# Kernel tuning notes

Measured on AMD Instinct MI355X. Metric: run time of the kernel, lower is better.

## Reference

```python
import jax, jax.numpy as jnp
import numpy as np

N_NODES = 100000
N_EDGES = 1600000
HEADS = 4
HID = 32
NEG_SLOPE = 0.2
EPS = 1e-16


def _gat_layer(x, w, a_src, a_dst, b, src, dst, n_nodes, concat):
    # x: [N, F_in], w: [H*C, F_in], a_src/a_dst: [H, C]
    H, C = a_src.shape
    h = (x @ w.T).reshape(-1, H, C)                      # [N, H, C]
    alpha_src = jnp.einsum('nhc,hc->nh', h, a_src)       # [N, H]
    alpha_dst = jnp.einsum('nhc,hc->nh', h, a_dst)       # [N, H]
    e = alpha_src[src] + alpha_dst[dst]                  # [E, H]
    e = jax.nn.leaky_relu(e, NEG_SLOPE)
    # segment softmax over incoming edges of each dst node
    m = jax.ops.segment_max(e, dst, num_segments=n_nodes)   # [N, H]
    ex = jnp.exp(e - m[dst])
    denom = jax.ops.segment_sum(ex, dst, num_segments=n_nodes)  # [N, H]
    alpha = ex / (denom[dst] + EPS)                      # [E, H]
    msg = alpha[:, :, None] * h[src]                     # [E, H, C]
    out = jax.ops.segment_sum(msg, dst, num_segments=n_nodes)  # [N, H, C]
    if concat:
        out = out.reshape(n_nodes, H * C)
    else:
        out = out.mean(axis=1)
    return out + b


def setup_inputs() -> dict:
    key = jax.random.key(0)
    ks = jax.random.split(key, 16)
    x = jax.random.normal(ks[0], (N_NODES, 3), dtype=jnp.float32)
    edge_index = jax.random.randint(ks[1], (2, N_EDGES), 0, N_NODES, dtype=jnp.int64 if jax.config.read('jax_enable_x64') else jnp.int32)
    s = 0.1
    return {
        'x': x,
        'edge_index': edge_index,
        'w1': jax.random.normal(ks[2], (HEADS * HID, 3)) * s,
        'att_src1': jax.random.normal(ks[3], (HEADS, HID)) * s,
        'att_dst1': jax.random.normal(ks[4], (HEADS, HID)) * s,
        'b1': jax.random.normal(ks[5], (HEADS * HID,)) * s,
        'w2': jax.random.normal(ks[6], (HID, HEADS * HID)) * s,
        'att_src2': jax.random.normal(ks[7], (1, HID)) * s,
        'att_dst2': jax.random.normal(ks[8], (1, HID)) * s,
        'b2': jax.random.normal(ks[9], (HID,)) * s,
        'mlp_w1': jax.random.normal(ks[10], (HID, 2 * HID)) * s,
        'mlp_b1': jax.random.normal(ks[11], (HID,)) * s,
        'mlp_w2': jax.random.normal(ks[12], (1, HID)) * s,
        'mlp_b2': jax.random.normal(ks[13], (1,)) * s,
    }


def reference(x, edge_index, w1, att_src1, att_dst1, b1, w2, att_src2, att_dst2, b2,
              mlp_w1, mlp_b1, mlp_w2, mlp_b2):
    src, dst = edge_index[0], edge_index[1]
    n = x.shape[0]
    # dropout layers are identity in eval mode
    h = _gat_layer(x, w1, att_src1, att_dst1, b1, src, dst, n, concat=True)   # [N, H*C]
    h = jax.nn.elu(h)
    h = _gat_layer(h, w2, att_src2, att_dst2, b2, src, dst, n, concat=False)  # [N, C]
    ef = jnp.concatenate([h[src], h[dst]], axis=-1)                            # [E, 2C]
    ef = jax.nn.relu(ef @ mlp_w1.T + mlp_b1)
    flows = (ef @ mlp_w2.T + mlp_b2).squeeze(-1)                               # [E]
    return jax.nn.relu(flows)
```

## Files before the change

### kernel.cpp

```cpp
#include <hip/hip_runtime.h>
#include <hip/hip_fp16.h>
#include <math.h>

#define N_NODES 100000
#define N_EDGES 1600000
#define NEG_SLOPE 0.2f
#define EPS 1e-16f

#define NBUCK 196
#define CHUNK 4096
#define BLKB 391

__device__ __forceinline__ float lrelu(float v) { return v > 0.f ? v : NEG_SLOPE * v; }

__device__ __forceinline__ float4 ld4h(const __half* p) {
    uint2 r = *(const uint2*)p;
    __half2 h0 = *reinterpret_cast<const __half2*>(&r.x);
    __half2 h1 = *reinterpret_cast<const __half2*>(&r.y);
    float2 f0 = __half22float2(h0), f1 = __half22float2(h1);
    return make_float4(f0.x, f0.y, f1.x, f1.y);
}

__device__ __forceinline__ void ld8h(const __half* p, float* f) {
    uint4 r = *(const uint4*)p;
    __half2 h0 = *reinterpret_cast<const __half2*>(&r.x);
    __half2 h1 = *reinterpret_cast<const __half2*>(&r.y);
    __half2 h2 = *reinterpret_cast<const __half2*>(&r.z);
    __half2 h3 = *reinterpret_cast<const __half2*>(&r.w);
    float2 f0 = __half22float2(h0), f1 = __half22float2(h1);
    float2 f2 = __half22float2(h2), f3 = __half22float2(h3);
    f[0] = f0.x; f[1] = f0.y; f[2] = f1.x; f[3] = f1.y;
    f[4] = f2.x; f[5] = f2.y; f[6] = f3.x; f[7] = f3.y;
}

__global__ void kA_hist(const int* __restrict__ ei, int* __restrict__ bh) {
    __shared__ int hist[NBUCK];
    int tid = threadIdx.x, b = blockIdx.x;
    if (tid < NBUCK) hist[tid] = 0;
    __syncthreads();
    int base = b * CHUNK;
    #pragma unroll
    for (int i = 0; i < CHUNK / 256; i++) {
        int e = base + i * 256 + tid;
        if (e < N_EDGES) {
            int dst = ei[N_EDGES + e];
            atomicAdd(&hist[dst >> 9], 1);
        }
    }
    __syncthreads();
    if (tid < NBUCK) bh[b * NBUCK + tid] = hist[tid];
}

__global__ void kS1(int* __restrict__ bh, int* __restrict__ bucketStart) {
    __shared__ int tsum[256];
    int k = blockIdx.x, t = threadIdx.x;
    int j0 = 2 * t, j1 = 2 * t + 1;
    int v0 = (j0 < BLKB) ? bh[j0 * NBUCK + k] : 0;
    int v1 = (j1 < BLKB) ? bh[j1 * NBUCK + k] : 0;
    int s = v0 + v1;
    tsum[t] = s;
    __syncthreads();
    for (int off = 1; off < 256; off <<= 1) {
        int tv = (t >= off) ? tsum[t - off] : 0;
        __syncthreads();
        tsum[t] += tv;
        __syncthreads();
    }
    int excl = tsum[t] - s;
    if (j0 < BLKB) bh[j0 * NBUCK + k] = excl;
    if (j1 < BLKB) bh[j1 * NBUCK + k] = excl + v0;
    if (t == 255) bucketStart[k] = tsum[255];
}

__global__ void kS2(int* __restrict__ bucketStart) {
    __shared__ int tmp[256];
    int t = threadIdx.x;
    int v = (t < NBUCK) ? bucketStart[t] : 0;
    tmp[t] = v;
    __syncthreads();
    for (int off = 1; off < 256; off <<= 1) {
        int tv = (t >= off) ? tmp[t - off] : 0;
        __syncthreads();
        tmp[t] += tv;
        __syncthreads();
    }
    if (t < NBUCK) bucketStart[t] = tmp[t] - v;
    if (t == NBUCK - 1) bucketStart[NBUCK] = tmp[t];
}

__global__ void kB_bin(const int* __restrict__ ei, const int* __restrict__ bh,
                       const int* __restrict__ bucketStart, int* __restrict__ binned) {
    __shared__ int cur[NBUCK];
    int tid = threadIdx.x, b = blockIdx.x;
    if (tid < NBUCK) cur[tid] = bucketStart[tid] + bh[b * NBUCK + tid];
    __syncthreads();
    int base = b * CHUNK;
    #pragma unroll
    for (int i = 0; i < CHUNK / 256; i++) {
        int e = base + i * 256 + tid;
        if (e < N_EDGES) {
            int src = ei[e], dst = ei[N_EDGES + e];
            int pos = atomicAdd(&cur[dst >> 9], 1);
            binned[pos] = src | ((dst & 511) << 17);
        }
    }
}

__global__ void kC_sort(const int* __restrict__ bucketStart, const int* __restrict__ binned,
                        int* __restrict__ deg, int* __restrict__ rowptr,
                        int* __restrict__ csr_src) {
    __shared__ int cnt[512];
    __shared__ int pfx[512];
    __shared__ int bsum[256];
    int t = threadIdx.x, k = blockIdx.x;
    int s0 = bucketStart[k], s1 = bucketStart[k + 1];
    cnt[t] = 0; cnt[t + 256] = 0;
    __syncthreads();
    for (int i = s0 + t; i < s1; i += 256)
        atomicAdd(&cnt[binned[i] >> 17], 1);
    __syncthreads();
    int a0 = cnt[2 * t], a1 = cnt[2 * t + 1];
    int s = a0 + a1;
    bsum[t] = s;
    __syncthreads();
    for (int off = 1; off < 256; off <<= 1) {
        int tv = (t >= off) ? bsum[t - off] : 0;
        __syncthreads();
        bsum[t] += tv;
        __syncthreads();
    }
    int excl = bsum[t] - s;
    pfx[2 * t] = excl;
    pfx[2 * t + 1] = excl + a0;
    int nb0 = k << 9;
    int n0 = nb0 + 2 * t, n1 = nb0 + 2 * t + 1;
    if (n0 < N_NODES) { deg[n0] = a0; rowptr[n0] = s0 + excl; }
    if (n1 < N_NODES) { deg[n1] = a1; rowptr[n1] = s0 + excl + a0; }
    __syncthreads();
    for (int i = s0 + t; i < s1; i += 256) {
        int pkd = binned[i];
        int pos = s0 + atomicAdd(&pfx[pkd >> 17], 1);
        csr_src[pos] = pkd & 0x1FFFF;
    }
}

__global__ void k_q(const float* __restrict__ w1, const float* __restrict__ as1,
                    const float* __restrict__ ad1, float* __restrict__ qv) {
    int t = threadIdx.x;
    if (t >= 24) return;
    int c = t % 3, h = (t / 3) % 4, side = t / 12;
    const float* att = side ? ad1 : as1;
    float acc = 0.f;
    for (int cc = 0; cc < 32; cc++)
        acc += att[h * 32 + cc] * w1[(h * 32 + cc) * 3 + c];
    qv[t] = acc;
}

__global__ void k_node1(const float* __restrict__ x, const float* __restrict__ qv,
                        float* __restrict__ a1d, float* __restrict__ p1) {
    int n = blockIdx.x * blockDim.x + threadIdx.x;
    if (n >= N_NODES) return;
    float x0 = x[n * 3], x1 = x[n * 3 + 1], x2 = x[n * 3 + 2];
    float4 s, d;
    s.x = x0 * qv[0]  + x1 * qv[1]  + x2 * qv[2];
    s.y = x0 * qv[3]  + x1 * qv[4]  + x2 * qv[5];
    s.z = x0 * qv[6]  + x1 * qv[7]  + x2 * qv[8];
    s.w = x0 * qv[9]  + x1 * qv[10] + x2 * qv[11];
    d.x = x0 * qv[12] + x1 * qv[13] + x2 * qv[14];
    d.y = x0 * qv[15] + x1 * qv[16] + x2 * qv[17];
    d.z = x0 * qv[18] + x1 * qv[19] + x2 * qv[20];
    d.w = x0 * qv[21] + x1 * qv[22] + x2 * qv[23];
    ((float4*)a1d)[n] = d;
    ((float4*)p1)[n * 2]     = s;
    float4 xx; xx.x = x0; xx.y = x1; xx.z = x2; xx.w = 1.f;
    ((float4*)p1)[n * 2 + 1] = xx;
}

#define G1_BLOCKS ((N_NODES + 31) / 32)
__global__ void k_gat1(const int* __restrict__ rowptr, const int* __restrict__ deg,
                       const int* __restrict__ csr_src,
                       const float* __restrict__ p1, const float* __restrict__ w1,
                       const float* __restrict__ a1d,
                       const float* __restrict__ b1, const float* __restrict__ w2,
                       const float* __restrict__ as2, const float* __restrict__ ad2,
                       __half* __restrict__ h2, float* __restrict__ a2s, float* __restrict__ a2d) {
    __shared__ float sm[32][16];
    __shared__ float f1s[4][128];
    int tid = threadIdx.x;
    int wave = tid >> 6, lane = tid & 63;
    int o = lane & 31, half = lane >> 5;
    int k0 = half * 64;

    int nl = wave * 8 + (lane >> 3);
    int ep = lane & 7;
    int n  = blockIdx.x * 32 + nl;
    if (n < N_NODES) {
        float4 ad4 = ((const float4*)a1d)[n];
        float adv0 = ad4.x, adv1 = ad4.y, adv2 = ad4.z, adv3 = ad4.w;
        int beg = rowptr[n], cnt = deg[n];
        float s0h[4] = {0.f, 0.f, 0.f, 0.f};
        float s1h[4] = {0.f, 0.f, 0.f, 0.f};
        float s2h[4] = {0.f, 0.f, 0.f, 0.f};
        float dnh[4] = {0.f, 0.f, 0.f, 0.f};
        int t = ep;
        int lim = cnt - 8;
        for (; t < lim; t += 16) {
            int i0 = csr_src[beg + t], i1 = csr_src[beg + t + 8];
            float4 A0 = ((const float4*)p1)[i0 * 2], X0 = ((const float4*)p1)[i0 * 2 + 1];
            float4 A1 = ((const float4*)p1)[i1 * 2], X1 = ((const float4*)p1)[i1 * 2 + 1];
            float av0[4] = {A0.x, A0.y, A0.z, A0.w};
            float av1[4] = {A1.x, A1.y, A1.z, A1.w};
            float ad_[4] = {adv0, adv1, adv2, adv3};
            #pragma unroll
            for (int hh = 0; hh < 4; hh++) {
                float e0 = __expf(lrelu(av0[hh] + ad_[hh]));
                float e1 = __expf(lrelu(av1[hh] + ad_[hh]));
                s0h[hh] += e0 * X0.x + e1 * X1.x;
                s1h[hh] += e0 * X0.y + e1 * X1.y;
                s2h[hh] += e0 * X0.z + e1 * X1.z;
                dnh[hh] += e0 + e1;
            }
        }
        for (; t < cnt; t += 8) {
            int i0 = csr_src[beg + t];
            float4 A0 = ((const float4*)p1)[i0 * 2], X0 = ((const float4*)p1)[i0 * 2 + 1];
            float av0[4] = {A0.x, A0.y, A0.z, A0.w};
            float ad_[4] = {adv0, adv1, adv2, adv3};
            #pragma unroll
            for (int hh = 0; hh < 4; hh++) {
                float e0 = __expf(lrelu(av0[hh] + ad_[hh]));
                s0h[hh] += e0 * X0.x;
                s1h[hh] += e0 * X0.y;
                s2h[hh] += e0 * X0.z;
                dnh[hh] += e0;
            }
        }
        #pragma unroll
        for (int hh = 0; hh < 4; hh++) {
            s0h[hh] += __shfl_xor(s0h[hh], 1); s0h[hh] += __shfl_xor(s0h[hh], 2); s0h[hh] += __shfl_xor(s0h[hh], 4);
            s1h[hh] += __shfl_xor(s1h[hh], 1); s1h[hh] += __shfl_xor(s1h[hh], 2); s1h[hh] += __shfl_xor(s1h[hh], 4);
            s2h[hh] += __shfl_xor(s2h[hh], 1); s2h[hh] += __shfl_xor(s2h[hh], 2); s2h[hh] += __shfl_xor(s2h[hh], 4);
            dnh[hh] += __shfl_xor(dnh[hh], 1); dnh[hh] += __shfl_xor(dnh[hh], 2); dnh[hh] += __shfl_xor(dnh[hh], 4);
        }
        if (ep < 4) {
            float4 r;
            r.x = ep == 0 ? s0h[0] : ep == 1 ? s0h[1] : ep == 2 ? s0h[2] : s0h[3];
            r.y = ep == 0 ? s1h[0] : ep == 1 ? s1h[1] : ep == 2 ? s1h[2] : s1h[3];
            r.z = ep == 0 ? s2h[0] : ep == 1 ? s2h[1] : ep == 2 ? s2h[2] : s2h[3];
            r.w = ep == 0 ? dnh[0] : ep == 1 ? dnh[1] : ep == 2 ? dnh[2] : dnh[3];
            *(float4*)&sm[nl][ep * 4] = r;
        }
    }

    float w2r[64];
    {
        const float4* wp = (const float4*)(w2 + o * 128 + k0);
        #pragma unroll
        for (int q = 0; q < 16; q++) {
            float4 t4 = wp[q];
            w2r[q * 4 + 0] = t4.x; w2r[q * 4 + 1] = t4.y;
            w2r[q * 4 + 2] = t4.z; w2r[q * 4 + 3] = t4.w;
        }
    }

    int j = lane, j2 = lane + 64;
    int h0 = j >> 5;
    float wa0 = w1[j * 3], wa1 = w1[j * 3 + 1], wa2 = w1[j * 3 + 2];
    float wb0 = w1[j2 * 3], wb1 = w1[j2 * 3 + 1], wb2 = w1[j2 * 3 + 2];
    float b1j = b1[j], b1j2 = b1[j2];
    float as2o = as2[o], ad2o = ad2[o];
    const float* f = f1s[wave];

    #pragma unroll 1
    for (int i = 0; i < 8; i++) {
        int n2 = blockIdx.x * 32 + wave * 8 + i;
        if (n2 >= N_NODES) break;
        const float* S = sm[wave * 8 + i];
        float v0 = (wa0 * S[h0 * 4] + wa1 * S[h0 * 4 + 1] + wa2 * S[h0 * 4 + 2])
                   / (S[h0 * 4 + 3] + EPS) + b1j;
        float v1 = (wb0 * S[(2 + h0) * 4] + wb1 * S[(2 + h0) * 4 + 1] + wb2 * S[(2 + h0) * 4 + 2])
                   / (S[(2 + h0) * 4 + 3] + EPS) + b1j2;
        f1s[wave][j]  = v0 > 0.f ? v0 : expm1f(v0);
        f1s[wave][j2] = v1 > 0.f ? v1 : expm1f(v1);
        float acc = 0.f;
        #pragma unroll
        for (int t = 0; t < 64; t++)
            acc += f[k0 + t] * w2r[t];
        acc += __shfl_down(acc, 32);
        if (half == 0) {
            h2[n2 * 32 + o] = __float2half(acc);
            float ps = acc * as2o, pd = acc * ad2o;
            #pragma unroll
            for (int off = 16; off; off >>= 1) {
                ps += __shfl_xor(ps, off);
                pd += __shfl_xor(pd, off);
            }
            if (o == 0) { a2s[n2] = ps; a2d[n2] = pd; }
        }
    }
}

#define G2_BLOCKS ((N_NODES + 15) / 16)
__global__ void k_gat2(const int* __restrict__ rowptr, const int* __restrict__ deg,
                       const int* __restrict__ csr_src,
                       const __half* __restrict__ h2, const float* __restrict__ a2s,
                       const float* __restrict__ a2d, const float* __restrict__ b2,
                       const float* __restrict__ mw1, const float* __restrict__ mb1,
                       __half* __restrict__ u, __half* __restrict__ v) {
    __shared__ float Ws2[2][32 * 36];
    __shared__ int2  pk[4][64];
    __shared__ float4 hfs[4][4][8];
    int tid = threadIdx.x;
    for (int i = tid; i < 2048; i += 256) {
        int c = i >> 6, col = i & 63;
        Ws2[col >> 5][c * 36 + (col & 31)] = mw1[i];
    }
    __syncthreads();
    int lane = tid & 63, w = tid >> 6;
    int nl = lane >> 4, sl = lane & 15;
    int eg2 = sl >> 2, qq = sl & 3;
    int n = blockIdx.x * 16 + w * 4 + nl;
    float4 b2a = ((const float4*)b2)[qq * 2];
    float4 b2b = ((const float4*)b2)[qq * 2 + 1];

    int beg = 0, cnt = 0;
    float ad = 0.f;
    if (n < N_NODES) { beg = rowptr[n]; cnt = deg[n]; ad = a2d[n]; }

    float acc[8] = {0.f, 0.f, 0.f, 0.f, 0.f, 0.f, 0.f, 0.f};
    float den = 0.f;
    int pkbase = (nl << 4);
    for (int b16 = 0; b16 < cnt; b16 += 16) {
        int li = b16 + sl;
        int idx = (li < cnt) ? csr_src[beg + li] : 0;
        float e = 0.f;
        if (li < cnt) e = __expf(lrelu(a2s[idx] + ad));
        den += e;
        pk[w][pkbase + sl] = make_int2(idx, __float_as_int(e));
        #pragma unroll
        for (int p = 0; p < 4; p++) {
            int2 pe = pk[w][pkbase + p * 4 + eg2];
            float g[8];
            ld8h(h2 + pe.x * 32 + qq * 8, g);
            float ee = __int_as_float(pe.y);
            acc[0] += ee * g[0]; acc[1] += ee * g[1];
            acc[2] += ee * g[2]; acc[3] += ee * g[3];
            acc[4] += ee * g[4]; acc[5] += ee * g[5];
            acc[6] += ee * g[6]; acc[7] += ee * g[7];
        }
    }
    #pragma unroll
    for (int j = 0; j < 8; j++) {
        float vv = acc[j];
        vv += __shfl_xor(vv, 4);
        vv += __shfl_xor(vv, 8);
        acc[j] = vv;
    }
    den += __shfl_xor(den, 1); den += __shfl_xor(den, 2);
    den += __shfl_xor(den, 4); den += __shfl_xor(den, 8);
    float inv = 1.f / (den + EPS);
    if (sl < 4) {
        float4 ha, hb;
        ha.x = acc[0] * inv + b2a.x; ha.y = acc[1] * inv + b2a.y;
        ha.z = acc[2] * inv + b2a.z; ha.w = acc[3] * inv + b2a.w;
        hb.x = acc[4] * inv + b2b.x; hb.y = acc[5] * inv + b2b.y;
        hb.z = acc[6] * inv + b2b.z; hb.w = acc[7] * inv + b2b.w;
        hfs[w][nl][qq * 2]     = ha;
        hfs[w][nl][qq * 2 + 1] = hb;
    }
    if (n < N_NODES) {
        int half_o = sl >> 3, c4 = (sl & 7) * 4;
        __half* outp = half_o ? v : u;
        float r0 = half_o ? 0.f : mb1[c4 + 0];
        float r1 = half_o ? 0.f : mb1[c4 + 1];
        float r2 = half_o ? 0.f : mb1[c4 + 2];
        float r3 = half_o ? 0.f : mb1[c4 + 3];
        const float* Wb = &Ws2[half_o][0];
        #pragma unroll
        for (int q = 0; q < 8; q++) {
            float4 hq = hfs[w][nl][q];
            float4 W0 = *(const float4*)&Wb[(c4 + 0) * 36 + q * 4];
            float4 W1 = *(const float4*)&Wb[(c4 + 1) * 36 + q * 4];
            float4 W2 = *(const float4*)&Wb[(c4 + 2) * 36 + q * 4];
            float4 W3 = *(const float4*)&Wb[(c4 + 3) * 36 + q * 4];
            r0 += W0.x * hq.x + W0.y * hq.y + W0.z * hq.z + W0.w * hq.w;
            r1 += W1.x * hq.x + W1.y * hq.y + W1.z * hq.z + W1.w * hq.w;
            r2 += W2.x * hq.x + W2.y * hq.y + W2.z * hq.z + W2.w * hq.w;
            r3 += W3.x * hq.x + W3.y * hq.y + W3.z * hq.z + W3.w * hq.w;
        }
        __half2 p0, p1;
        p0.x = __float2half(r0); p0.y = __float2half(r1);
        p1.x = __float2half(r2); p1.y = __float2half(r3);
        uint2 st;
        st.x = *reinterpret_cast<unsigned int*>(&p0);
        st.y = *reinterpret_cast<unsigned int*>(&p1);
        *reinterpret_cast<uint2*>(outp + n * 32 + c4) = st;
    }
}

#define MLP_BLOCKS 4096
__global__ void k_mlp(const int* __restrict__ ei, const __half* __restrict__ u,
                      const __half* __restrict__ v, const float* __restrict__ mw2,
                      const float* __restrict__ mb2, float* __restrict__ out) {
    int tid = threadIdx.x;
    int q = tid & 7;
    float4 w2q = ((const float4*)mw2)[q];
    float mb20 = mb2[0];
    int g = blockIdx.x * 32 + (tid >> 3);
    const int stride = MLP_BLOCKS * 32 * 4;
    for (int e = g * 4; e < N_EDGES; e += stride) {
        int eb = e;
        int e1 = (eb + 1 < N_EDGES) ? eb + 1 : eb;
        int e2 = (eb + 2 < N_EDGES) ? eb + 2 : eb;
        int e3 = (eb + 3 < N_EDGES) ? eb + 3 : eb;
        int sa = ei[eb], da = ei[N_EDGES + eb];
        int sb = ei[e1], db = ei[N_EDGES + e1];
        int sc = ei[e2], dc = ei[N_EDGES + e2];
        int sd = ei[e3], dd = ei[N_EDGES + e3];
        float4 ua = ld4h(u + sa * 32 + q * 4);
        float4 va = ld4h(v + da * 32 + q * 4);
        float4 ub = ld4h(u + sb * 32 + q * 4);
        float4 vb = ld4h(v + db * 32 + q * 4);
        float4 uc = ld4h(u + sc * 32 + q * 4);
        float4 vc = ld4h(v + dc * 32 + q * 4);
        float4 ud = ld4h(u + sd * 32 + q * 4);
        float4 vd = ld4h(v + dd * 32 + q * 4);
        float s0 = fmaxf(ua.x + va.x, 0.f) * w2q.x + fmaxf(ua.y + va.y, 0.f) * w2q.y
                 + fmaxf(ua.z + va.z, 0.f) * w2q.z + fmaxf(ua.w + va.w, 0.f) * w2q.w;
        float s1 = fmaxf(ub.x + vb.x, 0.f) * w2q.x + fmaxf(ub.y + vb.y, 0.f) * w2q.y
                 + fmaxf(ub.z + vb.z, 0.f) * w2q.z + fmaxf(ub.w + vb.w, 0.f) * w2q.w;
        float s2 = fmaxf(uc.x + vc.x, 0.f) * w2q.x + fmaxf(uc.y + vc.y, 0.f) * w2q.y
                 + fmaxf(uc.z + vc.z, 0.f) * w2q.z + fmaxf(uc.w + vc.w, 0.f) * w2q.w;
        float s3 = fmaxf(ud.x + vd.x, 0.f) * w2q.x + fmaxf(ud.y + vd.y, 0.f) * w2q.y
                 + fmaxf(ud.z + vd.z, 0.f) * w2q.z + fmaxf(ud.w + vd.w, 0.f) * w2q.w;
        s0 += __shfl_xor(s0, 1, 8); s0 += __shfl_xor(s0, 2, 8); s0 += __shfl_xor(s0, 4, 8);
        s1 += __shfl_xor(s1, 1, 8); s1 += __shfl_xor(s1, 2, 8); s1 += __shfl_xor(s1, 4, 8);
        s2 += __shfl_xor(s2, 1, 8); s2 += __shfl_xor(s2, 2, 8); s2 += __shfl_xor(s2, 4, 8);
        s3 += __shfl_xor(s3, 1, 8); s3 += __shfl_xor(s3, 2, 8); s3 += __shfl_xor(s3, 4, 8);
        if (q == 0) {
            out[eb] = fmaxf(s0 + mb20, 0.f);
            if (eb + 1 < N_EDGES) out[eb + 1] = fmaxf(s1 + mb20, 0.f);
            if (eb + 2 < N_EDGES) out[eb + 2] = fmaxf(s2 + mb20, 0.f);
            if (eb + 3 < N_EDGES) out[eb + 3] = fmaxf(s3 + mb20, 0.f);
        }
    }
}

extern "C" void kernel_launch(void* const* d_in, const int* in_sizes, int n_in,
                              void* d_out, int out_size, void* d_ws, size_t ws_size,
                              hipStream_t stream) {
    const float* x    = (const float*)d_in[0];
    const int*   ei   = (const int*)d_in[1];
    const float* w1   = (const float*)d_in[2];
    const float* as1  = (const float*)d_in[3];
    const float* ad1  = (const float*)d_in[4];
    const float* b1   = (const float*)d_in[5];
    const float* w2   = (const float*)d_in[6];
    const float* as2  = (const float*)d_in[7];
    const float* ad2  = (const float*)d_in[8];
    const float* b2   = (const float*)d_in[9];
    const float* mw1  = (const float*)d_in[10];
    const float* mb1  = (const float*)d_in[11];
    const float* mw2  = (const float*)d_in[12];
    const float* mb2  = (const float*)d_in[13];
    float* out = (float*)d_out;

    const int N = N_NODES;
    char* base   = (char*)d_ws;
    int* deg     = (int*)(base);
    int* rowptr  = (int*)(base + 400000);
    int* bstart  = (int*)(base + 800000);
    int* bh      = (int*)(base + 1200000);
    int* csr_src = (int*)(base + 1602048);
    float* p1    = (float*)(base + 8002048);
    float* a1d   = (float*)(base + 11202048);
    __half* h2   = (__half*)(base + 12802048);
    int* binned  = (int*)(base + 19202048);
    float* a2s   = (float*)(base + 25602048);
    float* a2d   = (float*)(base + 26002048);
    __half* u    = (__half*)(base + 26402048);
    __half* v    = (__half*)(base + 32802048);
    float* qv    = (float*)(base + 39202048);

    const int nb = (N + 255) / 256;

    kA_hist<<<BLKB, 256, 0, stream>>>(ei, bh);
    kS1<<<NBUCK, 256, 0, stream>>>(bh, bstart);
    kS2<<<1, 256, 0, stream>>>(bstart);
    kB_bin<<<BLKB, 256, 0, stream>>>(ei, bh, bstart, binned);
    kC_sort<<<NBUCK, 256, 0, stream>>>(bstart, binned, deg, rowptr, csr_src);

    k_q<<<1, 32, 0, stream>>>(w1, as1, ad1, qv);
    k_node1<<<nb, 256, 0, stream>>>(x, qv, a1d, p1);

    k_gat1<<<G1_BLOCKS, 256, 0, stream>>>(rowptr, deg, csr_src, p1, w1, a1d,
                                          b1, w2, as2, ad2, h2, a2s, a2d);

    k_gat2<<<G2_BLOCKS, 256, 0, stream>>>(rowptr, deg, csr_src, h2, a2s, a2d, b2,
                                          mw1, mb1, u, v);

    k_mlp<<<MLP_BLOCKS, 256, 0, stream>>>(ei, u, v, mw2, mb2, out);
}
```

Measured before the change: 283.0 us.

## Restructure GAT layer-1 kernel: 16 lanes per node, shared-memory W2 matvec

Reworks k_gat1 so each block handles 16 nodes with 16 lanes per node instead of 32 nodes with 8 lanes. Each lane computes 8 of the 128 layer-1 features in registers, and the 32x128 W2 projection now reads a padded copy of W2 staged in shared memory rather than 64 registers per thread. The change is meant to cut register pressure, raise edge-gather parallelism per node and remove the serial per-node loop. In exchange it adds a W2 load and a __syncthreads per block, doubles the block count and drops the 2-way edge unrolling.

```diff
diff --git a/kernel.cpp b/kernel.cpp
--- a/kernel.cpp
+++ b/kernel.cpp
@@ -176,7 +176,7 @@
     ((float4*)p1)[n * 2 + 1] = xx;
 }
 
-#define G1_BLOCKS ((N_NODES + 31) / 32)
+#define G1_BLOCKS ((N_NODES + 15) / 16)
 __global__ void k_gat1(const int* __restrict__ rowptr, const int* __restrict__ deg,
                        const int* __restrict__ csr_src,
                        const float* __restrict__ p1, const float* __restrict__ w1,
@@ -184,119 +184,113 @@
                        const float* __restrict__ b1, const float* __restrict__ w2,
                        const float* __restrict__ as2, const float* __restrict__ ad2,
                        __half* __restrict__ h2, float* __restrict__ a2s, float* __restrict__ a2d) {
-    __shared__ float sm[32][16];
-    __shared__ float f1s[4][128];
+    __shared__ float Ws[32 * 132];
+    __shared__ float F1[16][132];
     int tid = threadIdx.x;
-    int wave = tid >> 6, lane = tid & 63;
-    int o = lane & 31, half = lane >> 5;
-    int k0 = half * 64;
-
-    int nl = wave * 8 + (lane >> 3);
-    int ep = lane & 7;
-    int n  = blockIdx.x * 32 + nl;
+    for (int i = tid; i < 4096; i += 256) {
+        int o = i >> 7, k = i & 127;
+        Ws[o * 132 + k] = w2[i];
+    }
+    __syncthreads();
+    int lane = tid & 63, w = tid >> 6;
+    int nl = lane >> 4, sl = lane & 15;
+    int g = w * 4 + nl;
+    int n = blockIdx.x * 16 + g;
+
+    float w1r[24], b1r[8];
+    {
+        const float4* wp = (const float4*)(w1 + sl * 24);
+        #pragma unroll
+        for (int q = 0; q < 6; q++) {
+            float4 t4 = wp[q];
+            w1r[q * 4 + 0] = t4.x; w1r[q * 4 + 1] = t4.y;
+            w1r[q * 4 + 2] = t4.z; w1r[q * 4 + 3] = t4.w;
+        }
+        const float4* bp = (const float4*)(b1 + sl * 8);
+        float4 ta = bp[0], tb = bp[1];
+        b1r[0] = ta.x; b1r[1] = ta.y; b1r[2] = ta.z; b1r[3] = ta.w;
+        b1r[4] = tb.x; b1r[5] = tb.y; b1r[6] = tb.z; b1r[7] = tb.w;
+    }
+    float as2a = as2[sl], as2b = as2[sl + 16];
+    float ad2a = ad2[sl], ad2b = ad2[sl + 16];
+
+    float sA[4] = {0.f, 0.f, 0.f, 0.f};
+    float sB[4] = {0.f, 0.f, 0.f, 0.f};
+    float sC[4] = {0.f, 0.f, 0.f, 0.f};
+    float sD[4] = {0.f, 0.f, 0.f, 0.f};
     if (n < N_NODES) {
         float4 ad4 = ((const float4*)a1d)[n];
-        float adv0 = ad4.x, adv1 = ad4.y, adv2 = ad4.z, adv3 = ad4.w;
+        float adv[4] = {ad4.x, ad4.y, ad4.z, ad4.w};
         int beg = rowptr[n], cnt = deg[n];
-        float s0h[4] = {0.f, 0.f, 0.f, 0.f};
-        float s1h[4] = {0.f, 0.f, 0.f, 0.f};
-        float s2h[4] = {0.f, 0.f, 0.f, 0.f};
-        float dnh[4] = {0.f, 0.f, 0.f, 0.f};
-        int t = ep;
-        int lim = cnt - 8;
-        for (; t < lim; t += 16) {
-            int i0 = csr_src[beg + t], i1 = csr_src[beg + t + 8];
+        for (int t = sl; t < cnt; t += 16) {
+            int i0 = csr_src[beg + t];
             float4 A0 = ((const float4*)p1)[i0 * 2], X0 = ((const float4*)p1)[i0 * 2 + 1];
-            float4 A1 = ((const float4*)p1)[i1 * 2], X1 = ((const float4*)p1)[i1 * 2 + 1];
-            float av0[4] = {A0.x, A0.y, A0.z, A0.w};
-            float av1[4] = {A1.x, A1.y, A1.z, A1.w};
-            float ad_[4] = {adv0, adv1, adv2, adv3};
+            float av[4] = {A0.x, A0.y, A0.z, A0.w};
             #pragma unroll
             for (int hh = 0; hh < 4; hh++) {
-                float e0 = __expf(lrelu(av0[hh] + ad_[hh]));
-                float e1 = __expf(lrelu(av1[hh] + ad_[hh]));
-                s0h[hh] += e0 * X0.x + e1 * X1.x;
-                s1h[hh] += e0 * X0.y + e1 * X1.y;
-                s2h[hh] += e0 * X0.z + e1 * X1.z;
-                dnh[hh] += e0 + e1;
+                float e0 = __expf(lrelu(av[hh] + adv[hh]));
+                sA[hh] += e0 * X0.x;
+                sB[hh] += e0 * X0.y;
+                sC[hh] += e0 * X0.z;
+                sD[hh] += e0;
             }
         }
-        for (; t < cnt; t += 8) {
-            int i0 = csr_src[beg + t];
-            float4 A0 = ((const float4*)p1)[i0 * 2], X0 = ((const float4*)p1)[i0 * 2 + 1];
-            float av0[4] = {A0.x, A0.y, A0.z, A0.w};
-            float ad_[4] = {adv0, adv1, adv2, adv3};
-            #pragma unroll
-            for (int hh = 0; hh < 4; hh++) {
-                float e0 = __expf(lrelu(av0[hh] + ad_[hh]));
-                s0h[hh] += e0 * X0.x;
-                s1h[hh] += e0 * X0.y;
-                s2h[hh] += e0 * X0.z;
-                dnh[hh] += e0;
-            }
-        }
+    }
+    #pragma unroll
+    for (int hh = 0; hh < 4; hh++) {
+        sA[hh] += __shfl_xor(sA[hh], 1); sA[hh] += __shfl_xor(sA[hh], 2);
+        sA[hh] += __shfl_xor(sA[hh], 4); sA[hh] += __shfl_xor(sA[hh], 8);
+        sB[hh] += __shfl_xor(sB[hh], 1); sB[hh] += __shfl_xor(sB[hh], 2);
+        sB[hh] += __shfl_xor(sB[hh], 4); sB[hh] += __shfl_xor(sB[hh], 8);
+        sC[hh] += __shfl_xor(sC[hh], 1); sC[hh] += __shfl_xor(sC[hh], 2);
+        sC[hh] += __shfl_xor(sC[hh], 4); sC[hh] += __shfl_xor(sC[hh], 8);
+        sD[hh] += __shfl_xor(sD[hh], 1); sD[hh] += __shfl_xor(sD[hh], 2);
+        sD[hh] += __shfl_xor(sD[hh], 4); sD[hh] += __shfl_xor(sD[hh], 8);
+    }
+    {
+        int hh = sl >> 2;
+        float hs0 = hh == 0 ? sA[0] : hh == 1 ? sA[1] : hh == 2 ? sA[2] : sA[3];
+        float hs1 = hh == 0 ? sB[0] : hh == 1 ? sB[1] : hh == 2 ? sB[2] : sB[3];
+        float hs2 = hh == 0 ? sC[0] : hh == 1 ? sC[1] : hh == 2 ? sC[2] : sC[3];
+        float hsd = hh == 0 ? sD[0] : hh == 1 ? sD[1] : hh == 2 ? sD[2] : sD[3];
+        float inv = 1.f / (hsd + EPS);
+        float f1v[8];
         #pragma unroll
-        for (int hh = 0; hh < 4; hh++) {
-            s0h[hh] += __shfl_xor(s0h[hh], 1); s0h[hh] += __shfl_xor(s0h[hh], 2); s0h[hh] += __shfl_xor(s0h[hh], 4);
-            s1h[hh] += __shfl_xor(s1h[hh], 1); s1h[hh] += __shfl_xor(s1h[hh], 2); s1h[hh] += __shfl_xor(s1h[hh], 4);
-            s2h[hh] += __shfl_xor(s2h[hh], 1); s2h[hh] += __shfl_xor(s2h[hh], 2); s2h[hh] += __shfl_xor(s2h[hh], 4);
-            dnh[hh] += __shfl_xor(dnh[hh], 1); dnh[hh] += __shfl_xor(dnh[hh], 2); dnh[hh] += __shfl_xor(dnh[hh], 4);
-        }
-        if (ep < 4) {
-            float4 r;
-            r.x = ep == 0 ? s0h[0] : ep == 1 ? s0h[1] : ep == 2 ? s0h[2] : s0h[3];
-            r.y = ep == 0 ? s1h[0] : ep == 1 ? s1h[1] : ep == 2 ? s1h[2] : s1h[3];
-            r.z = ep == 0 ? s2h[0] : ep == 1 ? s2h[1] : ep == 2 ? s2h[2] : s2h[3];
-            r.w = ep == 0 ? dnh[0] : ep == 1 ? dnh[1] : ep == 2 ? dnh[2] : dnh[3];
-            *(float4*)&sm[nl][ep * 4] = r;
-        }
-    }
-
-    float w2r[64];
+        for (int i = 0; i < 8; i++) {
+            float vv = (w1r[i * 3] * hs0 + w1r[i * 3 + 1] * hs1 + w1r[i * 3 + 2] * hs2) * inv
+                       + b1r[i];
+            f1v[i] = vv > 0.f ? vv : expm1f(vv);
+        }
+        float4 fa, fb;
+        fa.x = f1v[0]; fa.y = f1v[1]; fa.z = f1v[2]; fa.w = f1v[3];
+        fb.x = f1v[4]; fb.y = f1v[5]; fb.z = f1v[6]; fb.w = f1v[7];
+        *(float4*)&F1[g][sl * 8]     = fa;
+        *(float4*)&F1[g][sl * 8 + 4] = fb;
+    }
+    float ra = 0.f, rb = 0.f;
     {
-        const float4* wp = (const float4*)(w2 + o * 128 + k0);
+        const float* Wa = &Ws[sl * 132];
+        const float* Wb = &Ws[(sl + 16) * 132];
+        const float* Fr = &F1[g][0];
         #pragma unroll
-        for (int q = 0; q < 16; q++) {
-            float4 t4 = wp[q];
-            w2r[q * 4 + 0] = t4.x; w2r[q * 4 + 1] = t4.y;
-            w2r[q * 4 + 2] = t4.z; w2r[q * 4 + 3] = t4.w;
-        }
-    }
-
-    int j = lane, j2 = lane + 64;
-    int h0 = j >> 5;
-    float wa0 = w1[j * 3], wa1 = w1[j * 3 + 1], wa2 = w1[j * 3 + 2];
-    float wb0 = w1[j2 * 3], wb1 = w1[j2 * 3 + 1], wb2 = w1[j2 * 3 + 2];
-    float b1j = b1[j], b1j2 = b1[j2];
-    float as2o = as2[o], ad2o = ad2[o];
-    const float* f = f1s[wave];
-
-    #pragma unroll 1
-    for (int i = 0; i < 8; i++) {
-        int n2 = blockIdx.x * 32 + wave * 8 + i;
-        if (n2 >= N_NODES) break;
-        const float* S = sm[wave * 8 + i];
-        float v0 = (wa0 * S[h0 * 4] + wa1 * S[h0 * 4 + 1] + wa2 * S[h0 * 4 + 2])
-                   / (S[h0 * 4 + 3] + EPS) + b1j;
-        float v1 = (wb0 * S[(2 + h0) * 4] + wb1 * S[(2 + h0) * 4 + 1] + wb2 * S[(2 + h0) * 4 + 2])
-                   / (S[(2 + h0) * 4 + 3] + EPS) + b1j2;
-        f1s[wave][j]  = v0 > 0.f ? v0 : expm1f(v0);
-        f1s[wave][j2] = v1 > 0.f ? v1 : expm1f(v1);
-        float acc = 0.f;
-        #pragma unroll
-        for (int t = 0; t < 64; t++)
-            acc += f[k0 + t] * w2r[t];
-        acc += __shfl_down(acc, 32);
-        if (half == 0) {
-            h2[n2 * 32 + o] = __float2half(acc);
-            float ps = acc * as2o, pd = acc * ad2o;
-            #pragma unroll
-            for (int off = 16; off; off >>= 1) {
-                ps += __shfl_xor(ps, off);
-                pd += __shfl_xor(pd, off);
-            }
-            if (o == 0) { a2s[n2] = ps; a2d[n2] = pd; }
-        }
+        for (int q = 0; q < 32; q++) {
+            float4 fq = *(const float4*)&Fr[q * 4];
+            float4 wa = *(const float4*)&Wa[q * 4];
+            float4 wb = *(const float4*)&Wb[q * 4];
+            ra += wa.x * fq.x + wa.y * fq.y + wa.z * fq.z + wa.w * fq.w;
+            rb += wb.x * fq.x + wb.y * fq.y + wb.z * fq.z + wb.w * fq.w;
+        }
+    }
+    if (n < N_NODES) {
+        h2[n * 32 + sl]      = __float2half(ra);
+        h2[n * 32 + sl + 16] = __float2half(rb);
+        float ps = ra * as2a + rb * as2b;
+        float pd = ra * ad2a + rb * ad2b;
+        ps += __shfl_xor(ps, 1); ps += __shfl_xor(ps, 2);
+        ps += __shfl_xor(ps, 4); ps += __shfl_xor(ps, 8);
+        pd += __shfl_xor(pd, 1); pd += __shfl_xor(pd, 2);
+        pd += __shfl_xor(pd, 4); pd += __shfl_xor(pd, 8);
+        if (sl == 0) { a2s[n] = ps; a2d[n] = pd; }
     }
 }
 
```

Measured after the change: 287.1 us. Within noise of the previous version (+1.4%).
